# Kernel optimization log

Hardware: AMD Instinct MI355X
Metric: run time of the kernel (lower is better)

The kernel has to match this reference:

```python
import jax, jax.numpy as jnp
import numpy as np

WS = 8       # window size
NH = 8       # heads
DIM = 256
HID = 512    # mlp hidden = dim * mlp_ratio
EPS = 1e-5


def _rel_pos_index(ws):
    coords = np.stack(np.meshgrid(np.arange(ws), np.arange(ws), indexing='ij')).reshape(2, -1)  # [2, N]
    rel = coords[:, :, None] - coords[:, None, :]          # [2, N, N]
    rel = rel.transpose(1, 2, 0).astype(np.int32)          # [N, N, 2]
    rel[..., 0] += ws - 1
    rel[..., 1] += ws - 1
    rel[..., 0] *= 2 * ws - 1
    return rel.sum(-1).reshape(-1)                          # [N*N]


def setup_inputs() -> dict:
    key = jax.random.key(0)
    ks = jax.random.split(key, 8)
    B, C, H, W = 8, DIM, 128, 128
    x = jax.random.normal(ks[0], (B, C, H, W), dtype=jnp.float32)
    s = 0.02
    return {
        'x': x,
        'ln1_g': jnp.ones((C,), jnp.float32),
        'ln1_b': jnp.zeros((C,), jnp.float32),
        'qkv_w': jax.random.normal(ks[1], (C, 3 * C), jnp.float32) * s,
        'qkv_b': jnp.zeros((3 * C,), jnp.float32),
        'proj_w': jax.random.normal(ks[2], (C, C), jnp.float32) * s,
        'proj_b': jnp.zeros((C,), jnp.float32),
        'rpb_table': jax.random.normal(ks[3], ((2 * WS - 1) ** 2, NH), jnp.float32) * s,
        'ln2_g': jnp.ones((C,), jnp.float32),
        'ln2_b': jnp.zeros((C,), jnp.float32),
        'w1': jax.random.normal(ks[4], (C, HID), jnp.float32) * s,
        'b1': jnp.zeros((HID,), jnp.float32),
        'w2': jax.random.normal(ks[5], (HID, C), jnp.float32) * s,
        'b2': jnp.zeros((C,), jnp.float32),
        'rpi': jnp.asarray(_rel_pos_index(WS)),
    }


def _ln(x, g, b):
    mu = x.mean(-1, keepdims=True)
    var = ((x - mu) ** 2).mean(-1, keepdims=True)
    return (x - mu) * jax.lax.rsqrt(var + EPS) * g + b


def reference(x, ln1_g, ln1_b, qkv_w, qkv_b, proj_w, proj_b, rpb_table,
              ln2_g, ln2_b, w1, b1, w2, b2, rpi):
    B, C, H, W = x.shape
    ws, nH = WS, NH
    hd = C // nH
    N = ws * ws
    scale = hd ** -0.5

    x_flat = x.reshape(B, C, H * W).transpose(0, 2, 1)      # [B, HW, C]
    shortcut = x_flat
    xn = _ln(x_flat, ln1_g, ln1_b)

    # window partition (H, W divisible by ws -> no padding)
    xw = xn.reshape(B, H // ws, ws, W // ws, ws, C)
    xw = xw.transpose(0, 1, 3, 2, 4, 5).reshape(-1, N, C)   # [Bw, N, C]

    qkv = (xw @ qkv_w + qkv_b).reshape(-1, N, 3, nH, hd)
    qkv = qkv.transpose(2, 0, 3, 1, 4)                       # [3, Bw, nH, N, hd]
    q, k, v = qkv[0], qkv[1], qkv[2]

    attn = jnp.einsum('bhnd,bhmd->bhnm', q, k) * scale       # [Bw, nH, N, N]
    bias = rpb_table[rpi].reshape(N, N, nH).transpose(2, 0, 1)
    attn = jax.nn.softmax(attn + bias[None], axis=-1)

    o = jnp.einsum('bhnm,bhmd->bhnd', attn, v)
    o = o.transpose(0, 2, 1, 3).reshape(-1, N, C)
    o = o @ proj_w + proj_b                                   # [Bw, N, C]

    # window reverse
    o = o.reshape(B, H // ws, W // ws, ws, ws, C)
    o = o.transpose(0, 1, 3, 2, 4, 5).reshape(B, H * W, C)

    x_flat = shortcut + o
    h = _ln(x_flat, ln2_g, ln2_b)
    h = jax.nn.gelu(h @ w1 + b1, approximate=False) @ w2 + b2
    x_flat = x_flat + h
    return x_flat.transpose(0, 2, 1).reshape(B, C, H, W)
```

## Files before the change

kernel.cpp:

```cpp
#include <hip/hip_runtime.h>
#include <cstdint>
#include <cstddef>

typedef unsigned short u16;
typedef __attribute__((ext_vector_type(4))) unsigned short u16x4;
typedef __attribute__((ext_vector_type(8))) short s16x8;
typedef __attribute__((ext_vector_type(4))) float f32x4;

__device__ __forceinline__ float b2f(u16 u) {
  union { unsigned int i; float f; } x; x.i = ((unsigned int)u) << 16; return x.f;
}
__device__ __forceinline__ u16 f2b(float f) {
  union { float f; unsigned int i; } x; x.f = f;
  unsigned int r = x.i + 0x7FFFu + ((x.i >> 16) & 1u);
  return (u16)(r >> 16);
}

__global__ __launch_bounds__(256) void zero_out(float* __restrict__ out) {
  size_t idx = ((size_t)blockIdx.x * 256 + threadIdx.x) * 4;
  f32x4 z = {0.f, 0.f, 0.f, 0.f};
  *(f32x4*)(out + idx) = z;
}


__global__ __launch_bounds__(256) void transp_w(const float* __restrict__ in, u16* __restrict__ out,
                                                int ksh, int N) {
  int idx = blockIdx.x * 256 + threadIdx.x;
  int K = 1 << ksh;
  if (idx >= K * N) return;
  int n = idx >> ksh;
  int k = idx & (K - 1);
  out[idx] = f2b(in[k * N + n]);
}

__global__ __launch_bounds__(256) void bias8_kernel(const float* __restrict__ rpb,
                                                    const int* __restrict__ rpi,
                                                    float* __restrict__ out) {
  int idx = blockIdx.x * 256 + threadIdx.x;
  int head = idx >> 12, pos = idx & 4095;
  out[idx] = rpb[rpi[pos] * 8 + head];
}

__global__ __launch_bounds__(256) void transpose_xc(const float* __restrict__ x, float* __restrict__ xf) {
  __shared__ float tile[64 * 65];
  int hw0 = blockIdx.x * 64;
  int c0 = blockIdx.y * 64;
  int lane = threadIdx.x & 63, grp = threadIdx.x >> 6;
  for (int cc = grp; cc < 64; cc += 4)
    tile[cc * 65 + lane] = x[((size_t)(c0 + cc) << 14) + hw0 + lane];
  __syncthreads();
  int j = threadIdx.x >> 2, cb = threadIdx.x & 3;
  float tmp[16];
  #pragma unroll
  for (int i = 0; i < 16; ++i) tmp[i] = tile[(cb * 16 + i) * 65 + j];
  float* dst = xf + ((size_t)(hw0 + j) << 8) + c0 + cb * 16;
  #pragma unroll
  for (int i = 0; i < 16; i += 4) *(f32x4*)(dst + i) = *(const f32x4*)(tmp + i);
}

__global__ __launch_bounds__(256) void ln_kernel(const float* __restrict__ xin,
                                                 const float* __restrict__ g,
                                                 const float* __restrict__ bb,
                                                 u16* __restrict__ out) {
  int wv = threadIdx.x >> 6, lane = threadIdx.x & 63;
  int t0 = blockIdx.x * 32 + wv * 8;
  f32x4 gv = *(const f32x4*)(g + lane * 4);
  f32x4 bv = *(const f32x4*)(bb + lane * 4);
  for (int it = 0; it < 8; ++it) {
    size_t base = ((size_t)(t0 + it) << 8) + lane * 4;
    f32x4 xv = *(const f32x4*)(xin + base);
    float s = 0.f, sq = 0.f;
    #pragma unroll
    for (int i = 0; i < 4; ++i) { s += xv[i]; sq += xv[i] * xv[i]; }
    #pragma unroll
    for (int m = 1; m < 64; m <<= 1) { s += __shfl_xor(s, m); sq += __shfl_xor(sq, m); }
    float mu = s * 0.00390625f;
    float var = sq * 0.00390625f - mu * mu;
    float rstd = rsqrtf(var + 1e-5f);
    u16x4 o;
    #pragma unroll
    for (int i = 0; i < 4; ++i) o[i] = f2b((xv[i] - mu) * rstd * gv[i] + bv[i]);
    *(u16x4*)(out + base) = o;
  }
}

__global__ __launch_bounds__(64) void attn_kernel(const u16* __restrict__ qkv,
                                                  const float* __restrict__ bias8,
                                                  u16* __restrict__ o) {
  __shared__ u16 vT[32 * 72];
  __shared__ u16 pS[64 * 72];
  int bid = blockIdx.x;
  int win = bid >> 3, head = bid & 7;
  int lane = threadIdx.x;
  int q = lane >> 4, l15 = lane & 15;
  int hb = (win >> 4) & 15, wb = win & 15;
  int tbase = hb * 8 * 128 + wb * 8;

  {
    int t = tbase + (lane >> 3) * 128 + (lane & 7);
    const u16* vrow = qkv + (size_t)t * 768 + 512 + head * 32;
    #pragma unroll
    for (int dq = 0; dq < 4; ++dq) {
      s16x8 vv = *(const s16x8*)(vrow + dq * 8);
      #pragma unroll
      for (int i = 0; i < 8; ++i) vT[(dq * 8 + i) * 72 + lane] = (u16)vv[i];
    }
  }

  s16x8 qf[4], kf[4];
  #pragma unroll
  for (int mt = 0; mt < 4; ++mt) {
    int m = mt * 16 + l15;
    int t = tbase + (m >> 3) * 128 + (m & 7);
    const u16* rowp = qkv + (size_t)t * 768 + head * 32 + q * 8;
    qf[mt] = *(const s16x8*)(rowp);
    kf[mt] = *(const s16x8*)(rowp + 256);
  }

  f32x4 S[4][4];
  #pragma unroll
  for (int mt = 0; mt < 4; ++mt)
    #pragma unroll
    for (int nt = 0; nt < 4; ++nt) {
      f32x4 z = {0.f, 0.f, 0.f, 0.f};
      S[mt][nt] = __builtin_amdgcn_mfma_f32_16x16x32_bf16(qf[mt], kf[nt], z, 0, 0, 0);
    }

  const float scale = 0.17677669529663689f;
  const float* bh = bias8 + head * 4096;
  float rinv[4][4];
  #pragma unroll
  for (int mt = 0; mt < 4; ++mt) {
    #pragma unroll
    for (int r = 0; r < 4; ++r) {
      int row = mt * 16 + q * 4 + r;
      float sv[4];
      float mx = -1e30f;
      #pragma unroll
      for (int nt = 0; nt < 4; ++nt) {
        int col = nt * 16 + l15;
        float v = S[mt][nt][r] * scale + bh[row * 64 + col];
        sv[nt] = v;
        mx = fmaxf(mx, v);
      }
      mx = fmaxf(mx, __shfl_xor(mx, 1));
      mx = fmaxf(mx, __shfl_xor(mx, 2));
      mx = fmaxf(mx, __shfl_xor(mx, 4));
      mx = fmaxf(mx, __shfl_xor(mx, 8));
      float sum = 0.f;
      #pragma unroll
      for (int nt = 0; nt < 4; ++nt) {
        float e = __expf(sv[nt] - mx);
        sum += e;
        S[mt][nt][r] = e;
      }
      sum += __shfl_xor(sum, 1);
      sum += __shfl_xor(sum, 2);
      sum += __shfl_xor(sum, 4);
      sum += __shfl_xor(sum, 8);
      rinv[mt][r] = 1.f / sum;
    }
  }

  #pragma unroll
  for (int mt = 0; mt < 4; ++mt)
    #pragma unroll
    for (int nt = 0; nt < 4; ++nt)
      #pragma unroll
      for (int r = 0; r < 4; ++r)
        pS[(mt * 16 + q * 4 + r) * 72 + nt * 16 + l15] = f2b(S[mt][nt][r]);
  __syncthreads();

  f32x4 O[4][2];
  #pragma unroll
  for (int mt = 0; mt < 4; ++mt)
    #pragma unroll
    for (int n2 = 0; n2 < 2; ++n2) O[mt][n2] = {0.f, 0.f, 0.f, 0.f};
  #pragma unroll
  for (int kt = 0; kt < 2; ++kt) {
    s16x8 vf[2];
    #pragma unroll
    for (int n2 = 0; n2 < 2; ++n2)
      vf[n2] = *(const s16x8*)(vT + (n2 * 16 + l15) * 72 + kt * 32 + q * 8);
    #pragma unroll
    for (int mt = 0; mt < 4; ++mt) {
      s16x8 pf = *(const s16x8*)(pS + (mt * 16 + l15) * 72 + kt * 32 + q * 8);
      #pragma unroll
      for (int n2 = 0; n2 < 2; ++n2)
        O[mt][n2] = __builtin_amdgcn_mfma_f32_16x16x32_bf16(pf, vf[n2], O[mt][n2], 0, 0, 0);
    }
  }
  #pragma unroll
  for (int mt = 0; mt < 4; ++mt)
    #pragma unroll
    for (int n2 = 0; n2 < 2; ++n2)
      #pragma unroll
      for (int r = 0; r < 4; ++r) {
        int row = mt * 16 + q * 4 + r;
        int col = n2 * 16 + l15;
        float v = O[mt][n2][r] * rinv[mt][r];
        o[((size_t)(win * 64 + row) << 8) + head * 32 + col] = f2b(v);
      }
}

template <int EPI>
__global__ __launch_bounds__(256) void gemm_k(const u16* __restrict__ A, const u16* __restrict__ BT,
                                              const float* __restrict__ bias, void* out_,
                                              const float* __restrict__ resid, int K, int N) {
  __shared__ u16 As[128 * 32];
  __shared__ u16 Bs[128 * 32];
  const int tid = threadIdx.x;
  const int wv = tid >> 6, lane = tid & 63;
  const int q = lane >> 4, l15 = lane & 15;
  const int m0 = blockIdx.x * 128, n0 = blockIdx.y * 128;
  const int wm = (wv & 1) * 64, wn = (wv >> 1) * 64;
  f32x4 acc[4][4] = {};

  const int srow = wv * 32 + (lane >> 2);
  const int scol = (lane & 3) * 8;
  const u16* Ag0 = A + (size_t)(m0 + srow) * K + scol;
  const u16* Ag1 = A + (size_t)(m0 + srow + 16) * K + scol;
  const u16* Bg0 = BT + (size_t)(n0 + srow) * K + scol;
  const u16* Bg1 = BT + (size_t)(n0 + srow + 16) * K + scol;
  u16* AsW0 = As + srow * 32 + scol;
  u16* AsW1 = As + (srow + 16) * 32 + scol;
  u16* BsW0 = Bs + srow * 32 + scol;
  u16* BsW1 = Bs + (srow + 16) * 32 + scol;

  for (int k0 = 0; k0 < K; k0 += 32) {
    s16x8 a0 = *(const s16x8*)(Ag0 + k0);
    s16x8 a1 = *(const s16x8*)(Ag1 + k0);
    s16x8 b0 = *(const s16x8*)(Bg0 + k0);
    s16x8 b1 = *(const s16x8*)(Bg1 + k0);
    *(s16x8*)AsW0 = a0;
    *(s16x8*)AsW1 = a1;
    *(s16x8*)BsW0 = b0;
    *(s16x8*)BsW1 = b1;
    __syncthreads();
    s16x8 af[4], bf[4];
    #pragma unroll
    for (int mt = 0; mt < 4; ++mt)
      af[mt] = *(const s16x8*)(As + (wm + mt * 16 + l15) * 32 + q * 8);
    #pragma unroll
    for (int nt = 0; nt < 4; ++nt)
      bf[nt] = *(const s16x8*)(Bs + (wn + nt * 16 + l15) * 32 + q * 8);
    #pragma unroll
    for (int mt = 0; mt < 4; ++mt)
      #pragma unroll
      for (int nt = 0; nt < 4; ++nt)
        acc[mt][nt] = __builtin_amdgcn_mfma_f32_16x16x32_bf16(af[mt], bf[nt], acc[mt][nt], 0, 0, 0);
    __syncthreads();
  }

  float bs[4];
  #pragma unroll
  for (int nt = 0; nt < 4; ++nt) bs[nt] = bias[n0 + wn + nt * 16 + l15];

  #pragma unroll
  for (int mt = 0; mt < 4; ++mt) {
    #pragma unroll
    for (int nt = 0; nt < 4; ++nt) {
      #pragma unroll
      for (int r = 0; r < 4; ++r) {
        int row = m0 + wm + mt * 16 + q * 4 + r;
        int col = n0 + wn + nt * 16 + l15;
        float v = acc[mt][nt][r] + bs[nt];
        if constexpr (EPI == 0) {
          ((u16*)out_)[(size_t)row * N + col] = f2b(v);
        } else if constexpr (EPI == 1) {
          int win = row >> 6, n = row & 63;
          int hb2 = (win >> 4) & 15, wb2 = win & 15;
          int t = ((hb2 * 8 + (n >> 3)) << 7) + wb2 * 8 + (n & 7);
          size_t idx = ((size_t)t << 8) + col;
          ((float*)out_)[idx] = v + resid[idx];
        } else if constexpr (EPI == 2) {
          v = 0.5f * v * (1.0f + erff(v * 0.70710678118654752f));
          ((u16*)out_)[(size_t)row * N + col] = f2b(v);
        } else {
          size_t ridx = ((size_t)row << 8) + col;
          v += resid[ridx];
          ((float*)out_)[(((size_t)col) << 14) + row] = v;
        }
      }
    }
  }
}

extern "C" void kernel_launch(void* const* d_in, const int* in_sizes, int n_in,
                              void* d_out, int out_size, void* d_ws, size_t ws_size,
                              hipStream_t stream) {
  const size_t NEEDED = 0x02920000;
  if (ws_size < NEEDED) {
    zero_out<<<dim3(32768), 256, 0, stream>>>((float*)d_out);
    return;
  }

  const float* x      = (const float*)d_in[0];
  const float* ln1_g  = (const float*)d_in[1];
  const float* ln1_b  = (const float*)d_in[2];
  const float* qkv_w  = (const float*)d_in[3];
  const float* qkv_b  = (const float*)d_in[4];
  const float* proj_w = (const float*)d_in[5];
  const float* proj_b = (const float*)d_in[6];
  const float* rpb    = (const float*)d_in[7];
  const float* ln2_g  = (const float*)d_in[8];
  const float* ln2_b  = (const float*)d_in[9];
  const float* w1     = (const float*)d_in[10];
  const float* b1     = (const float*)d_in[11];
  const float* w2     = (const float*)d_in[12];
  const float* b2     = (const float*)d_in[13];
  const int*   rpi    = (const int*)d_in[14];

  char* ws = (char*)d_ws;
  float* x2c   = (float*)(ws);
  u16*   qkvc  = (u16*)(ws + 0x01000000);
  u16*   h_inc = qkvc;
  u16*   h1c   = qkvc + 4194304;
  float* bias8 = (float*)(ws + 0x02800000);
  u16*   qkvT  = (u16*)(ws + 0x02820000);
  u16*   projT = (u16*)(ws + 0x02880000);
  u16*   w1T   = (u16*)(ws + 0x028A0000);
  u16*   w2T   = (u16*)(ws + 0x028E0000);

  transp_w<<<dim3(768), 256, 0, stream>>>(qkv_w, qkvT, 8, 768);
  transp_w<<<dim3(256), 256, 0, stream>>>(proj_w, projT, 8, 256);
  transp_w<<<dim3(512), 256, 0, stream>>>(w1, w1T, 8, 512);
  transp_w<<<dim3(512), 256, 0, stream>>>(w2, w2T, 9, 256);
  bias8_kernel<<<dim3(128), 256, 0, stream>>>(rpb, rpi, bias8);

  for (int b = 0; b < 8; ++b) {
    const float* xc   = x + (size_t)b * 4194304;
    float*       outc = (float*)d_out + (size_t)b * 4194304;
    u16*         xnc  = (u16*)outc;
    transpose_xc<<<dim3(256, 4), 256, 0, stream>>>(xc, x2c);
    ln_kernel<<<dim3(512), 256, 0, stream>>>(x2c, ln1_g, ln1_b, xnc);
    gemm_k<0><<<dim3(128, 6), 256, 0, stream>>>(xnc, qkvT, qkv_b, qkvc, nullptr, 256, 768);
    attn_kernel<<<dim3(2048), 64, 0, stream>>>(qkvc, bias8, xnc);
    gemm_k<1><<<dim3(128, 2), 256, 0, stream>>>(xnc, projT, proj_b, x2c, x2c, 256, 256);
    ln_kernel<<<dim3(512), 256, 0, stream>>>(x2c, ln2_g, ln2_b, h_inc);
    gemm_k<2><<<dim3(128, 4), 256, 0, stream>>>(h_inc, w1T, b1, h1c, nullptr, 256, 512);
    gemm_k<3><<<dim3(128, 2), 256, 0, stream>>>(h1c, w2T, b2, outc, x2c, 512, 256);
  }
}
```

Before: 1.176 ms.

## Batch multiple images per launch and use direct global-to-LDS loads in GEMM

Processes up to eight images per kernel launch, chosen by available workspace size, instead of looping over images one at a time. This gives larger grids and fewer launches, so there is less launch overhead and less GPU underutilisation. The GEMM tile staging now uses global_load_lds to copy straight into shared memory instead of going through registers, with an explicit vmcnt wait before the barrier. The cost is a larger workspace requirement, and the direct-to-LDS path depends on the LDS layout matching each wave's lane ordering.

```diff
diff --git a/kernel.cpp b/kernel.cpp
--- a/kernel.cpp
+++ b/kernel.cpp
@@ -7,14 +7,15 @@
 typedef __attribute__((ext_vector_type(8))) short s16x8;
 typedef __attribute__((ext_vector_type(4))) float f32x4;
 
-__device__ __forceinline__ float b2f(u16 u) {
-  union { unsigned int i; float f; } x; x.i = ((unsigned int)u) << 16; return x.f;
-}
 __device__ __forceinline__ u16 f2b(float f) {
   union { float f; unsigned int i; } x; x.f = f;
   unsigned int r = x.i + 0x7FFFu + ((x.i >> 16) & 1u);
   return (u16)(r >> 16);
 }
+
+#define GL16(gp, lp) __builtin_amdgcn_global_load_lds( \
+    (const __attribute__((address_space(1))) unsigned int*)(gp), \
+    (__attribute__((address_space(3))) unsigned int*)(lp), 16, 0, 0)
 
 __global__ __launch_bounds__(256) void zero_out(float* __restrict__ out) {
   size_t idx = ((size_t)blockIdx.x * 256 + threadIdx.x) * 4;
@@ -45,15 +46,17 @@
   __shared__ float tile[64 * 65];
   int hw0 = blockIdx.x * 64;
   int c0 = blockIdx.y * 64;
+  int b = blockIdx.z;
   int lane = threadIdx.x & 63, grp = threadIdx.x >> 6;
+  const float* xb = x + ((size_t)b << 22);
   for (int cc = grp; cc < 64; cc += 4)
-    tile[cc * 65 + lane] = x[((size_t)(c0 + cc) << 14) + hw0 + lane];
+    tile[cc * 65 + lane] = xb[((size_t)(c0 + cc) << 14) + hw0 + lane];
   __syncthreads();
   int j = threadIdx.x >> 2, cb = threadIdx.x & 3;
   float tmp[16];
   #pragma unroll
   for (int i = 0; i < 16; ++i) tmp[i] = tile[(cb * 16 + i) * 65 + j];
-  float* dst = xf + ((size_t)(hw0 + j) << 8) + c0 + cb * 16;
+  float* dst = xf + (((size_t)(b << 14) + hw0 + j) << 8) + c0 + cb * 16;
   #pragma unroll
   for (int i = 0; i < 16; i += 4) *(f32x4*)(dst + i) = *(const f32x4*)(tmp + i);
 }
@@ -93,8 +96,8 @@
   int win = bid >> 3, head = bid & 7;
   int lane = threadIdx.x;
   int q = lane >> 4, l15 = lane & 15;
-  int hb = (win >> 4) & 15, wb = win & 15;
-  int tbase = hb * 8 * 128 + wb * 8;
+  int b = win >> 8, hb = (win >> 4) & 15, wb = win & 15;
+  int tbase = (b << 14) + hb * 1024 + wb * 8;
 
   {
     int t = tbase + (lane >> 3) * 128 + (lane & 7);
@@ -222,20 +225,15 @@
   const u16* Ag1 = A + (size_t)(m0 + srow + 16) * K + scol;
   const u16* Bg0 = BT + (size_t)(n0 + srow) * K + scol;
   const u16* Bg1 = BT + (size_t)(n0 + srow + 16) * K + scol;
-  u16* AsW0 = As + srow * 32 + scol;
-  u16* AsW1 = As + (srow + 16) * 32 + scol;
-  u16* BsW0 = Bs + srow * 32 + scol;
-  u16* BsW1 = Bs + (srow + 16) * 32 + scol;
+  u16* AsW = As + wv * 32 * 32;
+  u16* BsW = Bs + wv * 32 * 32;
 
   for (int k0 = 0; k0 < K; k0 += 32) {
-    s16x8 a0 = *(const s16x8*)(Ag0 + k0);
-    s16x8 a1 = *(const s16x8*)(Ag1 + k0);
-    s16x8 b0 = *(const s16x8*)(Bg0 + k0);
-    s16x8 b1 = *(const s16x8*)(Bg1 + k0);
-    *(s16x8*)AsW0 = a0;
-    *(s16x8*)AsW1 = a1;
-    *(s16x8*)BsW0 = b0;
-    *(s16x8*)BsW1 = b1;
+    GL16(Ag0 + k0, AsW);
+    GL16(Ag1 + k0, AsW + 16 * 32);
+    GL16(Bg0 + k0, BsW);
+    GL16(Bg1 + k0, BsW + 16 * 32);
+    asm volatile("s_waitcnt vmcnt(0)" ::: "memory");
     __syncthreads();
     s16x8 af[4], bf[4];
     #pragma unroll
@@ -269,8 +267,8 @@
           ((u16*)out_)[(size_t)row * N + col] = f2b(v);
         } else if constexpr (EPI == 1) {
           int win = row >> 6, n = row & 63;
-          int hb2 = (win >> 4) & 15, wb2 = win & 15;
-          int t = ((hb2 * 8 + (n >> 3)) << 7) + wb2 * 8 + (n & 7);
+          int b = win >> 8, hb = (win >> 4) & 15, wb = win & 15;
+          int t = (b << 14) + ((hb * 8 + (n >> 3)) << 7) + wb * 8 + (n & 7);
           size_t idx = ((size_t)t << 8) + col;
           ((float*)out_)[idx] = v + resid[idx];
         } else if constexpr (EPI == 2) {
@@ -279,7 +277,8 @@
         } else {
           size_t ridx = ((size_t)row << 8) + col;
           v += resid[ridx];
-          ((float*)out_)[(((size_t)col) << 14) + row] = v;
+          int b = row >> 14, hw = row & 16383;
+          ((float*)out_)[(((size_t)(b * 256 + col)) << 14) + hw] = v;
         }
       }
     }
@@ -289,8 +288,13 @@
 extern "C" void kernel_launch(void* const* d_in, const int* in_sizes, int n_in,
                               void* d_out, int out_size, void* d_ws, size_t ws_size,
                               hipStream_t stream) {
-  const size_t NEEDED = 0x02920000;
-  if (ws_size < NEEDED) {
+  auto needed = [](int CB) -> size_t { return (size_t)CB * 0x02800000 + 0x120000; };
+  int CB;
+  if      (ws_size >= needed(8)) CB = 8;
+  else if (ws_size >= needed(4)) CB = 4;
+  else if (ws_size >= needed(2)) CB = 2;
+  else if (ws_size >= needed(1)) CB = 1;
+  else {
     zero_out<<<dim3(32768), 256, 0, stream>>>((float*)d_out);
     return;
   }
@@ -313,14 +317,15 @@
 
   char* ws = (char*)d_ws;
   float* x2c   = (float*)(ws);
-  u16*   qkvc  = (u16*)(ws + 0x01000000);
+  u16*   qkvc  = (u16*)(ws + (size_t)CB * 0x01000000);
   u16*   h_inc = qkvc;
-  u16*   h1c   = qkvc + 4194304;
-  float* bias8 = (float*)(ws + 0x02800000);
-  u16*   qkvT  = (u16*)(ws + 0x02820000);
-  u16*   projT = (u16*)(ws + 0x02880000);
-  u16*   w1T   = (u16*)(ws + 0x028A0000);
-  u16*   w2T   = (u16*)(ws + 0x028E0000);
+  u16*   h1c   = qkvc + (size_t)CB * 4194304;
+  char*  sm    = ws + (size_t)CB * 0x02800000;
+  float* bias8 = (float*)(sm);
+  u16*   qkvT  = (u16*)(sm + 0x20000);
+  u16*   projT = (u16*)(sm + 0x80000);
+  u16*   w1T   = (u16*)(sm + 0xA0000);
+  u16*   w2T   = (u16*)(sm + 0xE0000);
 
   transp_w<<<dim3(768), 256, 0, stream>>>(qkv_w, qkvT, 8, 768);
   transp_w<<<dim3(256), 256, 0, stream>>>(proj_w, projT, 8, 256);
@@ -328,17 +333,18 @@
   transp_w<<<dim3(512), 256, 0, stream>>>(w2, w2T, 9, 256);
   bias8_kernel<<<dim3(128), 256, 0, stream>>>(rpb, rpi, bias8);
 
-  for (int b = 0; b < 8; ++b) {
-    const float* xc   = x + (size_t)b * 4194304;
-    float*       outc = (float*)d_out + (size_t)b * 4194304;
+  const int nchunks = 8 / CB;
+  for (int c = 0; c < nchunks; ++c) {
+    const float* xc   = x + (size_t)c * CB * 4194304;
+    float*       outc = (float*)d_out + (size_t)c * CB * 4194304;
     u16*         xnc  = (u16*)outc;
-    transpose_xc<<<dim3(256, 4), 256, 0, stream>>>(xc, x2c);
-    ln_kernel<<<dim3(512), 256, 0, stream>>>(x2c, ln1_g, ln1_b, xnc);
-    gemm_k<0><<<dim3(128, 6), 256, 0, stream>>>(xnc, qkvT, qkv_b, qkvc, nullptr, 256, 768);
-    attn_kernel<<<dim3(2048), 64, 0, stream>>>(qkvc, bias8, xnc);
-    gemm_k<1><<<dim3(128, 2), 256, 0, stream>>>(xnc, projT, proj_b, x2c, x2c, 256, 256);
-    ln_kernel<<<dim3(512), 256, 0, stream>>>(x2c, ln2_g, ln2_b, h_inc);
-    gemm_k<2><<<dim3(128, 4), 256, 0, stream>>>(h_inc, w1T, b1, h1c, nullptr, 256, 512);
-    gemm_k<3><<<dim3(128, 2), 256, 0, stream>>>(h1c, w2T, b2, outc, x2c, 512, 256);
-  }
-}
+    transpose_xc<<<dim3(256, 4, CB), 256, 0, stream>>>(xc, x2c);
+    ln_kernel<<<dim3(CB * 512), 256, 0, stream>>>(x2c, ln1_g, ln1_b, xnc);
+    gemm_k<0><<<dim3(CB * 128, 6), 256, 0, stream>>>(xnc, qkvT, qkv_b, qkvc, nullptr, 256, 768);
+    attn_kernel<<<dim3(CB * 2048), 64, 0, stream>>>(qkvc, bias8, xnc);
+    gemm_k<1><<<dim3(CB * 128, 2), 256, 0, stream>>>(xnc, projT, proj_b, x2c, x2c, 256, 256);
+    ln_kernel<<<dim3(CB * 512), 256, 0, stream>>>(x2c, ln2_g, ln2_b, h_inc);
+    gemm_k<2><<<dim3(CB * 128, 4), 256, 0, stream>>>(h_inc, w1T, b1, h1c, nullptr, 256, 512);
+    gemm_k<3><<<dim3(CB * 128, 2), 256, 0, stream>>>(h1c, w2T, b2, outc, x2c, 512, 256);
+  }
+}
```

Measured after the change: 1.017 ms. 1.16x faster.
